# Performance work log

Measured on AMD Instinct MI355X. Metric: run time of the kernel, lower is better.

The kernel has to match this reference:

```python
import jax, jax.numpy as jnp
import numpy as np

NUM_EXPERTS = 8
TOP_K = 2
HIDDEN = 1024
INTER = 2048
TOKENS = 2048


def setup_inputs() -> dict:
    key = jax.random.key(0)
    k1, k2, k3, k4, k5 = jax.random.split(key, 5)
    inputs = jax.random.normal(k1, (TOKENS, HIDDEN), dtype=jnp.float32)
    router_logits = jax.random.normal(k2, (TOKENS, NUM_EXPERTS), dtype=jnp.float32)
    # expert weights, normal init (as nnx.initializers.normal -> stddev 0.01-ish; use 0.02)
    wi_0 = jax.random.normal(k3, (NUM_EXPERTS, HIDDEN, INTER), dtype=jnp.float32) * 0.02
    wi_1 = jax.random.normal(k4, (NUM_EXPERTS, HIDDEN, INTER), dtype=jnp.float32) * 0.02
    wo = jax.random.normal(k5, (NUM_EXPERTS, INTER, HIDDEN), dtype=jnp.float32) * 0.02
    return {"inputs": inputs, "router_logits": router_logits,
            "wi_0": wi_0, "wi_1": wi_1, "wo": wo}


def reference(inputs, router_logits, wi_0, wi_1, wo):
    T, H = inputs.shape
    E = wi_0.shape[0]
    K = TOP_K

    # --- routing: top-k + softmax over top-k logits (+ redundant renorm, as in source) ---
    top_k_logits, top_k_indices = jax.lax.top_k(router_logits, K)  # [T,K]
    w = jax.nn.softmax(top_k_logits, axis=-1)
    w = w / jnp.sum(w, axis=-1, keepdims=True)                      # [T,K]

    # --- permute: replicate each token K times, sort token-expert pairs by expert ---
    flat_experts = top_k_indices.reshape(-1)                        # [T*K], token-major
    sort_idx = jnp.argsort(flat_experts)                            # stable sort
    x_rep = jnp.repeat(inputs, K, axis=0)                           # [T*K, H]
    x_sorted = x_rep[sort_idx]                                      # rows grouped by expert
    group_sizes = jnp.bincount(flat_experts, length=E).astype(jnp.int32)  # [E]

    # --- grouped GEMM (ragged over contiguous expert groups): SwiGLU expert MLP ---
    h0 = jax.lax.ragged_dot(x_sorted, wi_0, group_sizes)            # [T*K, INTER]
    h1 = jax.lax.ragged_dot(x_sorted, wi_1, group_sizes)            # [T*K, INTER]
    inter = jax.nn.silu(h0) * h1
    y = jax.lax.ragged_dot(inter, wo, group_sizes)                  # [T*K, H]

    # --- unpermute + weighted combine ---
    y_unperm = jnp.zeros_like(y).at[sort_idx].set(y)                # back to token-major
    out = jnp.einsum('tkh,tk->th', y_unperm.reshape(T, K, H), w)
    return out
```

## Files before the change

kernel.cpp:

```cpp
#include <hip/hip_runtime.h>
#include <hip/hip_bf16.h>

#define T_TOKENS 2048
#define NE 8
#define HID 1024
#define INTER_ 2048
#define NPAIR (T_TOKENS * 2)

typedef unsigned short u16;
typedef __attribute__((ext_vector_type(4))) float f32x4;
typedef __attribute__((ext_vector_type(8))) short s16x8;

__device__ __forceinline__ u16 f2b(float f) {
    union { float f; unsigned u; } v; v.f = f;
    unsigned r = v.u + 0x7fffu + ((v.u >> 16) & 1u);
    return (u16)(r >> 16);
}

__device__ __forceinline__ void gl_lds16(const u16* g, u16* l) {
    __builtin_amdgcn_global_load_lds(
        (const __attribute__((address_space(1))) unsigned int*)g,
        (__attribute__((address_space(3))) unsigned int*)l, 16, 0, 0);
}

__global__ __launch_bounds__(256) void route_all(const float* __restrict__ logits,
                                                 int* __restrict__ offs,
                                                 int* __restrict__ pair_tok,
                                                 float* __restrict__ pair_w) {
    __shared__ int s_cnt[NE];
    __shared__ int s_cur[NE];
    __shared__ short s_e0[T_TOKENS];
    __shared__ short s_e1[T_TOKENS];
    __shared__ float s_w0[T_TOKENS];
    int tid = threadIdx.x;
    if (tid < NE) s_cnt[tid] = 0;
    __syncthreads();
    for (int t = tid; t < T_TOKENS; t += 256) {
        float l[NE];
#pragma unroll
        for (int i = 0; i < NE; i++) l[i] = logits[t * NE + i];
        int i0 = 0; float m0 = l[0];
#pragma unroll
        for (int i = 1; i < NE; i++) if (l[i] > m0) { m0 = l[i]; i0 = i; }
        int i1 = -1; float m1 = -1e30f;
#pragma unroll
        for (int i = 0; i < NE; i++) if (i != i0 && l[i] > m1) { m1 = l[i]; i1 = i; }
        float w0 = 1.f / (1.f + __expf(m1 - m0));
        s_e0[t] = (short)i0; s_e1[t] = (short)i1; s_w0[t] = w0;
        atomicAdd(&s_cnt[i0], 1);
        atomicAdd(&s_cnt[i1], 1);
    }
    __syncthreads();
    if (tid == 0) {
        int a = 0;
        for (int e = 0; e < NE; e++) { offs[e] = a; s_cur[e] = a; a += s_cnt[e]; }
        offs[NE] = a;
    }
    __syncthreads();
    for (int t = tid; t < T_TOKENS; t += 256) {
        int i0 = s_e0[t], i1 = s_e1[t];
        float w0 = s_w0[t];
        int sl0 = atomicAdd(&s_cur[i0], 1);
        pair_tok[sl0] = t; pair_w[sl0] = w0;
        int sl1 = atomicAdd(&s_cur[i1], 1);
        pair_tok[sl1] = t; pair_w[sl1] = 1.f - w0;
    }
}

__global__ void cvt_x_kernel(const float* __restrict__ x, u16* __restrict__ xb) {
    int i = blockIdx.x * 256 + threadIdx.x;
    float4 v = ((const float4*)x)[i];
    ushort4 b;
    b.x = f2b(v.x); b.y = f2b(v.y); b.z = f2b(v.z); b.w = f2b(v.w);
    ((ushort4*)xb)[i] = b;
}

__global__ __launch_bounds__(256) void transpose_all(const float* __restrict__ wi0,
                                                     const float* __restrict__ wi1,
                                                     const float* __restrict__ wo,
                                                     u16* __restrict__ wt0,
                                                     u16* __restrict__ wt1,
                                                     u16* __restrict__ wto) {
    int wsel = blockIdx.y >> 3, e = blockIdx.y & 7;
    const float* W; u16* Wt; int K, N, nb, kb;
    int bx = blockIdx.x;
    if (wsel == 0)      { W = wi0; Wt = wt0; }
    else if (wsel == 1) { W = wi1; Wt = wt1; }
    else                { W = wo;  Wt = wto; }
    if (wsel < 2) { K = HID; N = INTER_; nb = (bx & 31) * 64; kb = (bx >> 5) * 64; }
    else          { K = INTER_; N = HID; nb = (bx & 15) * 64; kb = (bx >> 4) * 64; }
    const float* Win = W + (size_t)e * K * N;
    u16* Wout = Wt + (size_t)e * N * K;
    __shared__ __align__(16) u16 tile[64 * 68];
    int tid = threadIdx.x;
#pragma unroll
    for (int p = 0; p < 4; p++) {
        int c = tid + p * 256;
        int r = c >> 4, c4 = c & 15;
        float4 v = *(const float4*)&Win[(size_t)(kb + r) * N + nb + c4 * 4];
        ushort4 b;
        b.x = f2b(v.x); b.y = f2b(v.y); b.z = f2b(v.z); b.w = f2b(v.w);
        *(ushort4*)&tile[r * 68 + c4 * 4] = b;
    }
    __syncthreads();
#pragma unroll
    for (int p = 0; p < 2; p++) {
        int k8 = p * 4 + (tid >> 6);
        int n = tid & 63;
        __align__(16) u16 tmp[8];
#pragma unroll
        for (int j = 0; j < 8; j++) tmp[j] = tile[(k8 * 8 + j) * 68 + n];
        *(uint4*)&Wout[(size_t)(nb + n) * K + kb + k8 * 8] = *(const uint4*)tmp;
    }
}

__global__ __launch_bounds__(256, 2) void fused_up_kernel(
        const u16* __restrict__ A, const u16* __restrict__ B0t, const u16* __restrict__ B1t,
        const int* __restrict__ pair_tok, const int* __restrict__ offs,
        u16* __restrict__ intr) {
    int e = blockIdx.z;
    int off = offs[e];
    int cnt = offs[e + 1] - off;
    int row0 = blockIdx.y * 128;
    if (row0 >= cnt) return;
    int nt = blockIdx.x * 128;

    __shared__ __align__(16) u16 As[128 * 64];
    __shared__ __align__(16) u16 Bs0[128 * 64];
    __shared__ __align__(16) u16 Bs1[128 * 64];

    int tid = threadIdx.x;
    int wave = tid >> 6, lane = tid & 63;

    const u16 *gA[4], *gB0[4], *gB1[4];
    u16 *lA[4], *lB0[4], *lB1[4];
    const size_t eNK = (size_t)e * INTER_ * HID;
#pragma unroll
    for (int is = 0; is < 4; is++) {
        int c = wave * 4 + is;
        int r = c * 8 + (lane >> 3);
        int sg = (lane & 7) ^ (r & 7);
        int mr = row0 + r; if (mr > cnt - 1) mr = cnt - 1;
        int arow = pair_tok[off + mr];
        gA[is]  = A + (size_t)arow * HID + sg * 8;
        gB0[is] = B0t + eNK + (size_t)(nt + r) * HID + sg * 8;
        gB1[is] = B1t + eNK + (size_t)(nt + r) * HID + sg * 8;
        lA[is]  = As  + c * 512;
        lB0[is] = Bs0 + c * 512;
        lB1[is] = Bs1 + c * 512;
    }

    int wr = (wave >> 1) * 64, wc = (wave & 1) * 64;
    int fm = lane & 15, quad = lane >> 4;

    f32x4 acc0[4][4], acc1[4][4];
#pragma unroll
    for (int i = 0; i < 4; i++)
#pragma unroll
        for (int j = 0; j < 4; j++) {
            acc0[i][j] = (f32x4){0.f, 0.f, 0.f, 0.f};
            acc1[i][j] = (f32x4){0.f, 0.f, 0.f, 0.f};
        }

    for (int kb = 0; kb < HID; kb += 64) {
#pragma unroll
        for (int is = 0; is < 4; is++) {
            gl_lds16(gA[is] + kb, lA[is]);
            gl_lds16(gB0[is] + kb, lB0[is]);
            gl_lds16(gB1[is] + kb, lB1[is]);
        }
        __syncthreads();
#pragma unroll
        for (int step = 0; step < 2; step++) {
            int f = step * 4 + quad;
            s16x8 af[4];
#pragma unroll
            for (int i = 0; i < 4; i++) {
                int R = wr + i * 16 + fm;
                af[i] = *(const s16x8*)&As[R * 64 + ((f ^ (R & 7)) * 8)];
            }
#pragma unroll
            for (int j = 0; j < 4; j++) {
                int R = wc + j * 16 + fm;
                s16x8 b0 = *(const s16x8*)&Bs0[R * 64 + ((f ^ (R & 7)) * 8)];
                s16x8 b1 = *(const s16x8*)&Bs1[R * 64 + ((f ^ (R & 7)) * 8)];
#pragma unroll
                for (int i = 0; i < 4; i++) {
                    acc0[i][j] = __builtin_amdgcn_mfma_f32_16x16x32_bf16(af[i], b0, acc0[i][j], 0, 0, 0);
                    acc1[i][j] = __builtin_amdgcn_mfma_f32_16x16x32_bf16(af[i], b1, acc1[i][j], 0, 0, 0);
                }
            }
        }
        __syncthreads();
    }

    int r4 = quad * 4, cc = lane & 15;
#pragma unroll
    for (int i = 0; i < 4; i++) {
#pragma unroll
        for (int reg = 0; reg < 4; reg++) {
            int rr = wr + i * 16 + r4 + reg;
            if (row0 + rr < cnt) {
                size_t slot = (size_t)(off + row0 + rr);
#pragma unroll
                for (int j = 0; j < 4; j++) {
                    int col = nt + wc + j * 16 + cc;
                    float a = acc0[i][j][reg];
                    float b = acc1[i][j][reg];
                    float s = a / (1.f + __expf(-a)) * b;
                    intr[slot * INTER_ + col] = f2b(s);
                }
            }
        }
    }
}

__global__ __launch_bounds__(256, 2) void down_kernel(
        const u16* __restrict__ A, const u16* __restrict__ Bt,
        const int* __restrict__ offs, const int* __restrict__ pair_tok,
        const float* __restrict__ pair_w, float* __restrict__ out) {
    int e = blockIdx.z >> 1, ks = blockIdx.z & 1;
    int off = offs[e];
    int cnt = offs[e + 1] - off;
    int row0 = blockIdx.y * 128;
    if (row0 >= cnt) return;
    int nt = blockIdx.x * 128;

    __shared__ __align__(16) u16 As[128 * 64];
    __shared__ __align__(16) u16 Bs[128 * 64];

    int tid = threadIdx.x;
    int wave = tid >> 6, lane = tid & 63;

    const u16 *gA[4], *gB[4];
    u16 *lA[4], *lB[4];
    const size_t eNK = (size_t)e * HID * INTER_;
#pragma unroll
    for (int is = 0; is < 4; is++) {
        int c = wave * 4 + is;
        int r = c * 8 + (lane >> 3);
        int sg = (lane & 7) ^ (r & 7);
        int mr = row0 + r; if (mr > cnt - 1) mr = cnt - 1;
        gA[is] = A + (size_t)(off + mr) * INTER_ + sg * 8;
        gB[is] = Bt + eNK + (size_t)(nt + r) * INTER_ + sg * 8;
        lA[is] = As + c * 512;
        lB[is] = Bs + c * 512;
    }

    int wr = (wave >> 1) * 64, wc = (wave & 1) * 64;
    int fm = lane & 15, quad = lane >> 4;

    f32x4 acc[4][4];
#pragma unroll
    for (int i = 0; i < 4; i++)
#pragma unroll
        for (int j = 0; j < 4; j++) acc[i][j] = (f32x4){0.f, 0.f, 0.f, 0.f};

    int kend = ks * 1024 + 1024;
    for (int kb = ks * 1024; kb < kend; kb += 64) {
#pragma unroll
        for (int is = 0; is < 4; is++) {
            gl_lds16(gA[is] + kb, lA[is]);
            gl_lds16(gB[is] + kb, lB[is]);
        }
        __syncthreads();
#pragma unroll
        for (int step = 0; step < 2; step++) {
            int f = step * 4 + quad;
            s16x8 af[4], bfr[4];
#pragma unroll
            for (int i = 0; i < 4; i++) {
                int R = wr + i * 16 + fm;
                af[i] = *(const s16x8*)&As[R * 64 + ((f ^ (R & 7)) * 8)];
            }
#pragma unroll
            for (int j = 0; j < 4; j++) {
                int R = wc + j * 16 + fm;
                bfr[j] = *(const s16x8*)&Bs[R * 64 + ((f ^ (R & 7)) * 8)];
            }
#pragma unroll
            for (int i = 0; i < 4; i++)
#pragma unroll
                for (int j = 0; j < 4; j++)
                    acc[i][j] = __builtin_amdgcn_mfma_f32_16x16x32_bf16(af[i], bfr[j], acc[i][j], 0, 0, 0);
        }
        __syncthreads();
    }

    int r4 = quad * 4, cc = lane & 15;
#pragma unroll
    for (int i = 0; i < 4; i++) {
#pragma unroll
        for (int reg = 0; reg < 4; reg++) {
            int rr = wr + i * 16 + r4 + reg;
            if (row0 + rr < cnt) {
                int slot = off + row0 + rr;
                int t = pair_tok[slot];
                float w = pair_w[slot];
#pragma unroll
                for (int j = 0; j < 4; j++) {
                    int col = nt + wc + j * 16 + cc;
                    atomicAdd(&out[(size_t)t * HID + col], w * acc[i][j][reg]);
                }
            }
        }
    }
}

extern "C" void kernel_launch(void* const* d_in, const int* in_sizes, int n_in,
                              void* d_out, int out_size, void* d_ws, size_t ws_size,
                              hipStream_t stream) {
    (void)in_sizes; (void)n_in; (void)ws_size;
    const float* x   = (const float*)d_in[0];
    const float* rl  = (const float*)d_in[1];
    const float* wi0 = (const float*)d_in[2];
    const float* wi1 = (const float*)d_in[3];
    const float* wo  = (const float*)d_in[4];
    float* out = (float*)d_out;

    char* p = (char*)d_ws;
    auto alloc = [&](size_t bytes) -> void* {
        void* r = (void*)p;
        p += (bytes + 255) & ~(size_t)255;
        return r;
    };
    u16* xb   = (u16*)alloc((size_t)T_TOKENS * HID * 2);
    u16* wt0  = (u16*)alloc((size_t)NE * HID * INTER_ * 2);
    u16* wt1  = (u16*)alloc((size_t)NE * HID * INTER_ * 2);
    u16* wto  = (u16*)alloc((size_t)NE * HID * INTER_ * 2);
    u16* intr = (u16*)alloc((size_t)NPAIR * INTER_ * 2);
    int* offs     = (int*)alloc((NE + 1) * sizeof(int));
    int* pair_tok = (int*)alloc(NPAIR * sizeof(int));
    float* pair_w = (float*)alloc(NPAIR * sizeof(float));

    hipMemsetAsync(out, 0, (size_t)out_size * sizeof(float), stream);
    route_all<<<1, 256, 0, stream>>>(rl, offs, pair_tok, pair_w);
    cvt_x_kernel<<<T_TOKENS * HID / 4 / 256, 256, 0, stream>>>(x, xb);
    transpose_all<<<dim3(512, 24), 256, 0, stream>>>(wi0, wi1, wo, wt0, wt1, wto);

    dim3 g1(INTER_ / 128, 16, NE);
    fused_up_kernel<<<g1, 256, 0, stream>>>(xb, wt0, wt1, pair_tok, offs, intr);
    dim3 g2(HID / 128, 16, NE * 2);
    down_kernel<<<g2, 256, 0, stream>>>(intr, wto, offs, pair_tok, pair_w, out);
}
```

Baseline: 349.2 us.

## Replace atomic scatter in down GEMM with partial buffers and combine kernel; vectorize transpose

The down-projection kernel now writes its split-K partial results as plain stores into a per-split, slot-ordered fp32 buffer instead of atomically adding weighted rows into the output. A new combine kernel gathers each token's two slots from both splits and applies the routing weights, and routing now records each token's slots and weights. This removes the output memset and the contended float atomics, at the cost of a larger workspace and extra global traffic for the partials. The weight transpose is also reworked so each thread loads a 4x4 block, transposes in registers and writes 16-byte vectors from LDS with a padded stride.

```diff
diff --git a/kernel.cpp b/kernel.cpp
--- a/kernel.cpp
+++ b/kernel.cpp
@@ -26,7 +26,9 @@
 __global__ __launch_bounds__(256) void route_all(const float* __restrict__ logits,
                                                  int* __restrict__ offs,
                                                  int* __restrict__ pair_tok,
-                                                 float* __restrict__ pair_w) {
+                                                 float* __restrict__ pair_w,
+                                                 int* __restrict__ pair_slot,
+                                                 float* __restrict__ tokW) {
     __shared__ int s_cnt[NE];
     __shared__ int s_cur[NE];
     __shared__ short s_e0[T_TOKENS];
@@ -62,8 +64,10 @@
         float w0 = s_w0[t];
         int sl0 = atomicAdd(&s_cur[i0], 1);
         pair_tok[sl0] = t; pair_w[sl0] = w0;
+        pair_slot[2 * t] = sl0; tokW[2 * t] = w0;
         int sl1 = atomicAdd(&s_cur[i1], 1);
         pair_tok[sl1] = t; pair_w[sl1] = 1.f - w0;
+        pair_slot[2 * t + 1] = sl1; tokW[2 * t + 1] = 1.f - w0;
     }
 }
 
@@ -75,6 +79,7 @@
     ((ushort4*)xb)[i] = b;
 }
 
+#define TSTR 72
 __global__ __launch_bounds__(256) void transpose_all(const float* __restrict__ wi0,
                                                      const float* __restrict__ wi1,
                                                      const float* __restrict__ wo,
@@ -91,26 +96,33 @@
     else          { K = INTER_; N = HID; nb = (bx & 15) * 64; kb = (bx >> 4) * 64; }
     const float* Win = W + (size_t)e * K * N;
     u16* Wout = Wt + (size_t)e * N * K;
-    __shared__ __align__(16) u16 tile[64 * 68];
+    __shared__ __align__(16) u16 tile[64 * TSTR];
     int tid = threadIdx.x;
-#pragma unroll
-    for (int p = 0; p < 4; p++) {
-        int c = tid + p * 256;
-        int r = c >> 4, c4 = c & 15;
-        float4 v = *(const float4*)&Win[(size_t)(kb + r) * N + nb + c4 * 4];
-        ushort4 b;
-        b.x = f2b(v.x); b.y = f2b(v.y); b.z = f2b(v.z); b.w = f2b(v.w);
-        *(ushort4*)&tile[r * 68 + c4 * 4] = b;
+    {
+        int n4 = (tid & 15) * 4;
+        int k4 = (tid >> 4) * 4;
+        float4 v[4];
+#pragma unroll
+        for (int j = 0; j < 4; j++)
+            v[j] = *(const float4*)&Win[(size_t)(kb + k4 + j) * N + nb + n4];
+#pragma unroll
+        for (int i = 0; i < 4; i++) {
+            ushort4 o;
+            o.x = f2b(((const float*)&v[0])[i]);
+            o.y = f2b(((const float*)&v[1])[i]);
+            o.z = f2b(((const float*)&v[2])[i]);
+            o.w = f2b(((const float*)&v[3])[i]);
+            *(ushort4*)&tile[(n4 + i) * TSTR + k4] = o;
+        }
     }
     __syncthreads();
-#pragma unroll
-    for (int p = 0; p < 2; p++) {
-        int k8 = p * 4 + (tid >> 6);
-        int n = tid & 63;
-        __align__(16) u16 tmp[8];
-#pragma unroll
-        for (int j = 0; j < 8; j++) tmp[j] = tile[(k8 * 8 + j) * 68 + n];
-        *(uint4*)&Wout[(size_t)(nb + n) * K + kb + k8 * 8] = *(const uint4*)tmp;
+    {
+        int n = tid >> 2, ks = tid & 3;
+#pragma unroll
+        for (int c = 0; c < 2; c++) {
+            uint4 v = *(const uint4*)&tile[n * TSTR + ks * 8 + 32 * c];
+            *(uint4*)&Wout[(size_t)(nb + n) * K + kb + ks * 8 + 32 * c] = v;
+        }
     }
 }
 
@@ -217,8 +229,7 @@
 
 __global__ __launch_bounds__(256, 2) void down_kernel(
         const u16* __restrict__ A, const u16* __restrict__ Bt,
-        const int* __restrict__ offs, const int* __restrict__ pair_tok,
-        const float* __restrict__ pair_w, float* __restrict__ out) {
+        const int* __restrict__ offs, float* __restrict__ ypart) {
     int e = blockIdx.z >> 1, ks = blockIdx.z & 1;
     int off = offs[e];
     int cnt = offs[e + 1] - off;
@@ -288,29 +299,48 @@
     }
 
     int r4 = quad * 4, cc = lane & 15;
+    float* yout = ypart + (size_t)ks * NPAIR * HID;
 #pragma unroll
     for (int i = 0; i < 4; i++) {
 #pragma unroll
         for (int reg = 0; reg < 4; reg++) {
             int rr = wr + i * 16 + r4 + reg;
             if (row0 + rr < cnt) {
-                int slot = off + row0 + rr;
-                int t = pair_tok[slot];
-                float w = pair_w[slot];
+                size_t slot = (size_t)(off + row0 + rr);
 #pragma unroll
                 for (int j = 0; j < 4; j++) {
                     int col = nt + wc + j * 16 + cc;
-                    atomicAdd(&out[(size_t)t * HID + col], w * acc[i][j][reg]);
+                    yout[slot * HID + col] = acc[i][j][reg];
                 }
             }
         }
     }
+}
+
+__global__ void combine_kernel(const float* __restrict__ y0, const float* __restrict__ y1,
+                               const int* __restrict__ pair_slot,
+                               const float* __restrict__ tokW, float* __restrict__ out) {
+    int i = blockIdx.x * 256 + threadIdx.x;
+    int t = i >> 8;
+    int h4 = i & 255;
+    int s0 = pair_slot[2 * t], s1 = pair_slot[2 * t + 1];
+    float w0 = tokW[2 * t], w1 = tokW[2 * t + 1];
+    float4 a0 = ((const float4*)y0)[(size_t)s0 * 256 + h4];
+    float4 a1 = ((const float4*)y1)[(size_t)s0 * 256 + h4];
+    float4 b0 = ((const float4*)y0)[(size_t)s1 * 256 + h4];
+    float4 b1 = ((const float4*)y1)[(size_t)s1 * 256 + h4];
+    float4 r;
+    r.x = w0 * (a0.x + a1.x) + w1 * (b0.x + b1.x);
+    r.y = w0 * (a0.y + a1.y) + w1 * (b0.y + b1.y);
+    r.z = w0 * (a0.z + a1.z) + w1 * (b0.z + b1.z);
+    r.w = w0 * (a0.w + a1.w) + w1 * (b0.w + b1.w);
+    ((float4*)out)[i] = r;
 }
 
 extern "C" void kernel_launch(void* const* d_in, const int* in_sizes, int n_in,
                               void* d_out, int out_size, void* d_ws, size_t ws_size,
                               hipStream_t stream) {
-    (void)in_sizes; (void)n_in; (void)ws_size;
+    (void)in_sizes; (void)n_in; (void)out_size; (void)ws_size;
     const float* x   = (const float*)d_in[0];
     const float* rl  = (const float*)d_in[1];
     const float* wi0 = (const float*)d_in[2];
@@ -329,17 +359,21 @@
     u16* wt1  = (u16*)alloc((size_t)NE * HID * INTER_ * 2);
     u16* wto  = (u16*)alloc((size_t)NE * HID * INTER_ * 2);
     u16* intr = (u16*)alloc((size_t)NPAIR * INTER_ * 2);
+    float* ypart = (float*)alloc((size_t)2 * NPAIR * HID * 4);
     int* offs     = (int*)alloc((NE + 1) * sizeof(int));
     int* pair_tok = (int*)alloc(NPAIR * sizeof(int));
     float* pair_w = (float*)alloc(NPAIR * sizeof(float));
-
-    hipMemsetAsync(out, 0, (size_t)out_size * sizeof(float), stream);
-    route_all<<<1, 256, 0, stream>>>(rl, offs, pair_tok, pair_w);
+    int* pair_slot= (int*)alloc(NPAIR * sizeof(int));
+    float* tokW   = (float*)alloc(NPAIR * sizeof(float));
+
+    route_all<<<1, 256, 0, stream>>>(rl, offs, pair_tok, pair_w, pair_slot, tokW);
     cvt_x_kernel<<<T_TOKENS * HID / 4 / 256, 256, 0, stream>>>(x, xb);
     transpose_all<<<dim3(512, 24), 256, 0, stream>>>(wi0, wi1, wo, wt0, wt1, wto);
 
     dim3 g1(INTER_ / 128, 16, NE);
     fused_up_kernel<<<g1, 256, 0, stream>>>(xb, wt0, wt1, pair_tok, offs, intr);
     dim3 g2(HID / 128, 16, NE * 2);
-    down_kernel<<<g2, 256, 0, stream>>>(intr, wto, offs, pair_tok, pair_w, out);
-}
+    down_kernel<<<g2, 256, 0, stream>>>(intr, wto, offs, ypart);
+    combine_kernel<<<T_TOKENS * HID / 4 / 256, 256, 0, stream>>>(
+        ypart, ypart + (size_t)NPAIR * HID, pair_slot, tokW, out);
+}
```

Result: faster. 331.0 us (-5.2%).
